# Performance work log

Hardware: AMD Instinct MI355X
Metric: run time of the kernel (lower is better)

The kernel has to match this reference:

```python
import jax, jax.numpy as jnp
import numpy as np

N = 50000            # num nodes
E = 800000           # num edges
IN_CH = 128          # memory_dim (node feature dim)
OUT_CH = 128         # out_channels (4 heads x 32)
HEADS = 4
HEAD_DIM = OUT_CH // HEADS
TIME_DIM = 100
MSG_DIM = 1
EDGE_DIM = TIME_DIM + MSG_DIM
T_MAX = 1_000_000


def _glorot(k, shape):
    lim = (6.0 / (shape[0] + shape[1])) ** 0.5
    return jax.random.uniform(k, shape, jnp.float32, -lim, lim)


def setup_inputs() -> dict:
    key = jax.random.key(0)
    ks = jax.random.split(key, 16)
    return {
        "x": jax.random.normal(ks[0], (N, IN_CH), jnp.float32),
        "msg": jax.random.normal(ks[1], (E, MSG_DIM), jnp.float32),
        # TimeEncoder: Linear(1, time_dim) followed by cos
        "Wt": _glorot(ks[2], (1, TIME_DIM)),
        "bt": jnp.zeros((TIME_DIM,), jnp.float32),
        # TransformerConv projections (stored [in, out])
        "Wq": _glorot(ks[3], (IN_CH, OUT_CH)),
        "bq": jnp.zeros((OUT_CH,), jnp.float32),
        "Wk": _glorot(ks[4], (IN_CH, OUT_CH)),
        "bk": jnp.zeros((OUT_CH,), jnp.float32),
        "Wv": _glorot(ks[5], (IN_CH, OUT_CH)),
        "bv": jnp.zeros((OUT_CH,), jnp.float32),
        "We": _glorot(ks[6], (EDGE_DIM, OUT_CH)),   # lin_edge, bias=False
        "Wskip": _glorot(ks[7], (IN_CH, OUT_CH)),    # lin_skip (root weight)
        "bskip": jnp.zeros((OUT_CH,), jnp.float32),
        # LayerNorm params
        "gamma": jnp.ones((OUT_CH,), jnp.float32),
        "beta": jnp.zeros((OUT_CH,), jnp.float32),
        # int inputs
        "last_update": jax.random.randint(ks[8], (N,), 0, T_MAX, jnp.int64 if jax.config.jax_enable_x64 else jnp.int32),
        "edge_index": jax.random.randint(ks[9], (2, E), 0, N, jnp.int32),
        "t": jax.random.randint(ks[10], (E,), 0, T_MAX, jnp.int64 if jax.config.jax_enable_x64 else jnp.int32),
    }


def reference(x, msg, Wt, bt, Wq, bq, Wk, bk, Wv, bv, We, Wskip, bskip, gamma, beta,
              last_update, edge_index, t):
    src, dst = edge_index[0], edge_index[1]  # PyG: row=source j, col=target i

    # edge features: cos-time encoding of relative time, concat raw message
    rel_t = (last_update[src] - t).astype(jnp.float32)[:, None]        # [E,1]
    rel_t_enc = jnp.cos(rel_t @ Wt + bt)                               # [E,time_dim]
    edge_attr = jnp.concatenate([rel_t_enc, msg], axis=-1)             # [E,edge_dim]

    # TransformerConv (heads=4, per-head dim=32, concat=True, root_weight=True)
    q = (x @ Wq + bq)[dst].reshape(E, HEADS, HEAD_DIM)
    k = (x @ Wk + bk)[src].reshape(E, HEADS, HEAD_DIM)
    v = (x @ Wv + bv)[src].reshape(E, HEADS, HEAD_DIM)
    e = (edge_attr @ We).reshape(E, HEADS, HEAD_DIM)

    kj = k + e
    alpha = jnp.einsum('ehd,ehd->eh', q, kj) / jnp.sqrt(jnp.float32(HEAD_DIM))  # [E,H]

    # segment (scatter) softmax over incoming edges of each destination node
    m = jax.lax.stop_gradient(jax.ops.segment_max(alpha, dst, num_segments=N))  # [N,H]
    ea = jnp.exp(alpha - m[dst])
    den = jax.ops.segment_sum(ea, dst, num_segments=N)                          # [N,H]
    a = ea / (den[dst] + 1e-16)                                                  # [E,H]

    msg_e = (v + e) * a[..., None]                                               # [E,H,D]
    agg = jax.ops.segment_sum(msg_e.reshape(E, OUT_CH), dst, num_segments=N)     # [N,out]

    out = agg + (x @ Wskip + bskip)   # skip / root weight
    out = jax.nn.relu(out)

    # LayerNorm
    mu = out.mean(-1, keepdims=True)
    var = out.var(-1, keepdims=True)
    return (out - mu) * jax.lax.rsqrt(var + 1e-5) * gamma + beta
```

## Files before the change

### kernel.cpp

```cpp
#include <hip/hip_runtime.h>
#include <math.h>

#define NN 50000
#define NE 800000
#define TDIM 100
#define MAXCH 100000
#define NBLK 196

typedef _Float16 half2v __attribute__((ext_vector_type(2)));
typedef _Float16 half4v __attribute__((ext_vector_type(4)));
typedef _Float16 half8v __attribute__((ext_vector_type(8)));
typedef __fp16 fp16x2 __attribute__((ext_vector_type(2)));
typedef float f32x4 __attribute__((ext_vector_type(4)));

union U16 { uint4 u; half8v h; };
union U4h { unsigned u; half2v h; };

__device__ __forceinline__ float ref_cosf(float x) {
  const float C1 = 0.15915494f;
  const float C2 = 6.42063831e-9f;
  float p = x * C1;
  float r = __fmaf_rn(x, C1, -p);
  r = __fmaf_rn(x, C2, r);
  float n = rintf(p);
  float f = (p - n) + r;
  return __builtin_amdgcn_cosf(f);
}

__device__ __forceinline__ unsigned pk16(float a, float b) {
  fp16x2 h = __builtin_amdgcn_cvt_pkrtz(a, b);
  unsigned u;
  __builtin_memcpy(&u, &h, 4);
  return u;
}

__device__ __forceinline__ float fdot2f(unsigned a, unsigned b, float c) {
  U4h ua, ub; ua.u = a; ub.u = b;
#if __has_builtin(__builtin_amdgcn_fdot2)
  return __builtin_amdgcn_fdot2(ua.h, ub.h, c, false);
#else
  return c + (float)ua.h.x * (float)ub.h.x + (float)ua.h.y * (float)ub.h.y;
#endif
}

__device__ __forceinline__ unsigned pkadd(unsigned a, unsigned b) {
  half2v x, y; __builtin_memcpy(&x, &a, 4); __builtin_memcpy(&y, &b, 4);
  half2v z = x + y; unsigned r; __builtin_memcpy(&r, &z, 4); return r;
}
__device__ __forceinline__ unsigned pkmul(unsigned a, unsigned b) {
  half2v x, y; __builtin_memcpy(&x, &a, 4); __builtin_memcpy(&y, &b, 4);
  half2v z = x * y; unsigned r; __builtin_memcpy(&r, &z, 4); return r;
}

template<int CTRL>
__device__ __forceinline__ int dpp_i(int x) {
  return __builtin_amdgcn_update_dpp(0, x, CTRL, 0xf, 0xf, true);
}
template<int CTRL>
__device__ __forceinline__ float dpp_addf(float x) {
  return x + __int_as_float(dpp_i<CTRL>(__float_as_int(x)));
}
template<int CTRL>
__device__ __forceinline__ float dpp_maxf(float x) {
  return fmaxf(x, __int_as_float(dpp_i<CTRL>(__float_as_int(x))));
}
__device__ __forceinline__ float red16_add(float x) {
  x = dpp_addf<0xB1>(x); x = dpp_addf<0x4E>(x);
  x = dpp_addf<0x141>(x); x = dpp_addf<0x140>(x);
  return x;
}
__device__ __forceinline__ float red16_max(float x) {
  x = dpp_maxf<0xB1>(x); x = dpp_maxf<0x4E>(x);
  x = dpp_maxf<0x141>(x); x = dpp_maxf<0x140>(x);
  return x;
}
__device__ __forceinline__ unsigned red16_pkadd(unsigned x) {
  x = pkadd(x, (unsigned)dpp_i<0xB1>((int)x));
  x = pkadd(x, (unsigned)dpp_i<0x4E>((int)x));
  x = pkadd(x, (unsigned)dpp_i<0x141>((int)x));
  x = pkadd(x, (unsigned)dpp_i<0x140>((int)x));
  return x;
}

__device__ __forceinline__ void build_bfu(float rel_b, float mg_b, int g,
                                          const float2* wtbt_s, unsigned bfu[4][4]) {
#pragma unroll
  for (int ks = 0; ks < 4; ++ks) {
#pragma unroll
    for (int p = 0; p < 4; ++p) {
      int j0 = ks * 32 + g * 8 + 2 * p;
      float a0 = 0.f, a1 = 0.f;
      if (ks < 3) {
        float2 w0 = wtbt_s[j0], w1 = wtbt_s[j0 + 1];
        a0 = ref_cosf(__fmaf_rn(rel_b, w0.x, w0.y));
        a1 = ref_cosf(__fmaf_rn(rel_b, w1.x, w1.y));
      } else {
        if (j0 < 100) {
          float2 w0 = wtbt_s[j0];
          a0 = ref_cosf(__fmaf_rn(rel_b, w0.x, w0.y));
        } else if (j0 == 100) a0 = mg_b;
        if (j0 + 1 < 100) {
          float2 w1 = wtbt_s[j0 + 1];
          a1 = ref_cosf(__fmaf_rn(rel_b, w1.x, w1.y));
        } else if (j0 + 1 == 100) a1 = mg_b;
      }
      bfu[ks][p] = pk16(a0, a1);
    }
  }
}

__global__ void k_init(const float* __restrict__ We,
                       const float* __restrict__ Wq, const float* __restrict__ Wk,
                       const float* __restrict__ Wv, const float* __restrict__ Wskip,
                       uint4* __restrict__ wef, uint4* __restrict__ wpf,
                       const int* __restrict__ ei, int* __restrict__ deg) {
  int idx = blockIdx.x * 256 + threadIdx.x;
  if (idx < 2048) {
    int lane = idx & 63, fi = idx >> 6;
    int ks = fi >> 3, mt = fi & 7;
    int ch = mt * 16 + (lane & 15);
    int k0 = ks * 32 + ((lane >> 4) << 3);
    U16 cv;
#pragma unroll
    for (int jj = 0; jj < 8; ++jj) {
      int j = k0 + jj;
      cv.h[jj] = (j <= 100) ? (_Float16)We[j * 128 + ch] : (_Float16)0.f;
    }
    wef[idx] = cv.u;
  } else if (idx < 2048 + 8192) {
    int i2 = idx - 2048;
    int lane = i2 & 63, fi = i2 >> 6;
    int nt = fi & 7, ks = (fi >> 3) & 3, cy = fi >> 5;
    const float* W = (cy == 0) ? Wq : (cy == 1) ? Wk : (cy == 2) ? Wv : Wskip;
    int n = nt * 16 + (lane & 15);
    int k0 = ks * 32 + ((lane >> 4) << 3);
    U16 cv;
#pragma unroll
    for (int jj = 0; jj < 8; ++jj)
      cv.h[jj] = (_Float16)W[(k0 + jj) * 128 + n];
    wpf[i2] = cv.u;
  }
  if (idx < NE) atomicAdd(&deg[ei[NE + idx]], 1);
}

__global__ __launch_bounds__(256) void k_proj2(
    const float* __restrict__ x,
    const float* __restrict__ bq, const float* __restrict__ bk,
    const float* __restrict__ bv, const float* __restrict__ bskip,
    const uint4* __restrict__ wpf,
    _Float16* __restrict__ Q16, _Float16* __restrict__ K16,
    _Float16* __restrict__ V16, _Float16* __restrict__ S16)
{
  __shared__ unsigned xs[32][68];
  __shared__ _Float16 os[32][136];

  const int cy = blockIdx.x;
  const int n0 = blockIdx.y * 32;
  const int tid = threadIdx.x;
  const float* bias = (cy == 0) ? bq : (cy == 1) ? bk : (cy == 2) ? bv : bskip;
  _Float16* dst     = (cy == 0) ? Q16 : (cy == 1) ? K16 : (cy == 2) ? V16 : S16;

  {
    int r = tid >> 3, c16 = (tid & 7) * 16;
    int row = n0 + r;
    float4 v0 = {0,0,0,0}, v1 = {0,0,0,0}, v2 = {0,0,0,0}, v3 = {0,0,0,0};
    if (row < NN) {
      const float4* xp = (const float4*)&x[(size_t)row * 128 + c16];
      v0 = xp[0]; v1 = xp[1]; v2 = xp[2]; v3 = xp[3];
    }
    unsigned* xr = &xs[r][c16 >> 1];
    xr[0] = pk16(v0.x, v0.y); xr[1] = pk16(v0.z, v0.w);
    xr[2] = pk16(v1.x, v1.y); xr[3] = pk16(v1.z, v1.w);
    xr[4] = pk16(v2.x, v2.y); xr[5] = pk16(v2.z, v2.w);
    xr[6] = pk16(v3.x, v3.y); xr[7] = pk16(v3.z, v3.w);
  }
  __syncthreads();

  const int w = tid >> 6, lane = tid & 63;
  const int mrow = (w & 1) << 4;
  const int nh = w >> 1;

  f32x4 acc[4] = {{0,0,0,0},{0,0,0,0},{0,0,0,0},{0,0,0,0}};
#pragma unroll
  for (int ks = 0; ks < 4; ++ks) {
    U16 a_; a_.u = *(const uint4*)&xs[mrow + (lane & 15)][ks * 16 + ((lane >> 4) << 2)];
#pragma unroll
    for (int nt = 0; nt < 4; ++nt) {
      U16 b_; b_.u = wpf[((cy * 4 + ks) * 8 + nh * 4 + nt) * 64 + lane];
      acc[nt] = __builtin_amdgcn_mfma_f32_16x16x32_f16(a_.h, b_.h, acc[nt], 0, 0, 0);
    }
  }

#pragma unroll
  for (int nt = 0; nt < 4; ++nt) {
    int col = (nh * 4 + nt) * 16 + (lane & 15);
    float bb = bias[col];
    int rbase = mrow + ((lane >> 4) << 2);
#pragma unroll
    for (int reg = 0; reg < 4; ++reg)
      os[rbase + reg][col] = (_Float16)(acc[nt][reg] + bb);
  }
  __syncthreads();

  {
    int r = tid >> 3, c16 = (tid & 7) * 16;
    int row = n0 + r;
    if (row < NN) {
      const _Float16* op = &os[r][c16];
      if (cy < 3) {
#pragma unroll
        for (int q = 0; q < 4; ++q) {
          int j4 = (c16 >> 2) + q;
          int po = ((j4 & 3) << 5) | ((j4 >> 2) << 2);
          *(half4v*)&dst[(size_t)row * 128 + po] = *(const half4v*)&op[q * 4];
        }
      } else {
        *(uint4*)&dst[(size_t)row * 128 + c16]     = ((const uint4*)op)[0];
        *(uint4*)&dst[(size_t)row * 128 + c16 + 8] = ((const uint4*)op)[1];
      }
    }
  }
}

__global__ __launch_bounds__(256) void k_scan1(const int* __restrict__ deg,
                                               int* __restrict__ off,
                                               int* __restrict__ choff,
                                               int* __restrict__ bsum,
                                               int* __restrict__ bsumc) {
  __shared__ int s[256], sc[256];
  const int b = blockIdx.x, t = threadIdx.x;
  const int n = b * 256 + t;
  int d = (n < NN) ? deg[n] : 0;
  int c = (d + 15) >> 4;
  s[t] = d; sc[t] = c;
  __syncthreads();
  for (int o = 1; o < 256; o <<= 1) {
    int v1 = 0, v2 = 0;
    if (t >= o) { v1 = s[t - o]; v2 = sc[t - o]; }
    __syncthreads();
    if (t >= o) { s[t] += v1; sc[t] += v2; }
    __syncthreads();
  }
  if (n < NN) { off[n] = s[t] - d; choff[n] = sc[t] - c; }
  if (t == 255) { bsum[b] = s[255]; bsumc[b] = sc[255]; }
}

__global__ __launch_bounds__(256) void k_scan2(int* __restrict__ bsum,
                                               int* __restrict__ bsumc,
                                               int* __restrict__ off,
                                               int* __restrict__ choff) {
  __shared__ int s[256], sc[256];
  const int t = threadIdx.x;
  int v = (t < NBLK) ? bsum[t] : 0;
  int vc = (t < NBLK) ? bsumc[t] : 0;
  s[t] = v; sc[t] = vc;
  __syncthreads();
  for (int o = 1; o < 256; o <<= 1) {
    int v1 = 0, v2 = 0;
    if (t >= o) { v1 = s[t - o]; v2 = sc[t - o]; }
    __syncthreads();
    if (t >= o) { s[t] += v1; sc[t] += v2; }
    __syncthreads();
  }
  if (t < NBLK) { bsum[t] = s[t] - v; bsumc[t] = sc[t] - vc; }
  if (t == 255) { off[NN] = s[255]; choff[NN] = sc[255]; }
}

__global__ void k_scan3(int* __restrict__ off, int* __restrict__ choff,
                        const int* __restrict__ bsum, const int* __restrict__ bsumc) {
  int b = blockIdx.x, n = b * 256 + threadIdx.x;
  if (n < NN) { off[n] += bsum[b]; choff[n] += bsumc[b]; }
}

__global__ void k_fillch(const int* __restrict__ ei, const int* __restrict__ deg,
                         const int* __restrict__ off, const int* __restrict__ choff,
                         int* __restrict__ cur, int* __restrict__ elist,
                         uint2* __restrict__ chunks) {
  int b = blockIdx.x;
  if (b < 3125) {
    int e = b * 256 + threadIdx.x;
    if (e < NE) {
      int d = ei[NE + e];
      int p = atomicAdd(&cur[d], 1);
      elist[off[d] + p] = e;
    }
  } else {
    int n = (b - 3125) * 256 + threadIdx.x;
    if (n < NN) {
      int d = deg[n], o = off[n], c = choff[n];
      int nch = (d + 15) >> 4;
      for (int j = 0; j < nch; ++j) {
        int cnt = d - 16 * j; if (cnt > 16) cnt = 16;
        chunks[c + j] = make_uint2((unsigned)(o + 16 * j),
                                   ((unsigned)n << 5) | (unsigned)cnt);
      }
    }
  }
}

__global__ __launch_bounds__(512) void k_edge(
    const _Float16* __restrict__ Q16, const _Float16* __restrict__ K16,
    const _Float16* __restrict__ V16,
    const float* __restrict__ Wt, const float* __restrict__ bt,
    const uint4* __restrict__ wefrag,
    const float* __restrict__ msg, const int* __restrict__ last_update,
    const int* __restrict__ ei, const int* __restrict__ tt,
    const int* __restrict__ elist, const uint2* __restrict__ chunks,
    const int* __restrict__ choff,
    unsigned* __restrict__ numbuf, float4* __restrict__ mdm,
    float4* __restrict__ mdd)
{
  __shared__ uint4 wef_s[2048];
  __shared__ float2 wtbt_s[104];
  __shared__ unsigned accs_u[8][64];

  for (int i = threadIdx.x; i < 2048; i += 512) wef_s[i] = wefrag[i];
  if (threadIdx.x < 104) {
    int j = threadIdx.x;
    wtbt_s[j] = make_float2(j < TDIM ? Wt[j] : 0.f, j < TDIM ? bt[j] : 0.f);
  }
  __syncthreads();

  const int wid = threadIdx.x >> 6, lane = threadIdx.x & 63;
  const int chunk = blockIdx.x * 8 + wid;
  if (chunk >= choff[NN]) return;

  uint2 ce = chunks[chunk];
  const int estart = (int)ce.x;
  const int node = (int)(ce.y >> 5);
  const int cnt = (int)(ce.y & 31u);
  const int g = lane >> 4, ed = lane & 15;

  const int edc = (ed < cnt) ? ed : (cnt - 1);
  const int eid = elist[estart + edc];
  const int src_b = ei[eid];
  const float mg_b = msg[eid];
  const float rel_b = (float)(last_update[src_b] - tt[eid]);
  const bool valid = (ed < cnt);

  unsigned bfu[4][4];
  build_bfu(rel_b, mg_b, g, wtbt_s, bfu);

  f32x4 ec[8];
#pragma unroll
  for (int mt = 0; mt < 8; ++mt) {
    f32x4 c4 = {0.f, 0.f, 0.f, 0.f};
#pragma unroll
    for (int ks = 0; ks < 4; ++ks) {
      U16 av2; av2.u = wef_s[(ks * 8 + mt) * 64 + lane];
      U16 bv2; bv2.u.x = bfu[ks][0]; bv2.u.y = bfu[ks][1];
      bv2.u.z = bfu[ks][2]; bv2.u.w = bfu[ks][3];
      c4 = __builtin_amdgcn_mfma_f32_16x16x32_f16(av2.h, bv2.h, c4, 0, 0, 0);
    }
    ec[mt] = c4;
  }

  unsigned ep2[16];
#pragma unroll
  for (int mt = 0; mt < 8; ++mt) {
    ep2[mt * 2 + 0] = pk16(ec[mt][0], ec[mt][1]);
    ep2[mt * 2 + 1] = pk16(ec[mt][2], ec[mt][3]);
  }

  float pal[4];
  {
    const uint4* qp = (const uint4*)&Q16[(size_t)node * 128 + g * 32];
    const uint4* kp = (const uint4*)&K16[(size_t)src_b * 128 + g * 32];
#pragma unroll
    for (int i = 0; i < 4; ++i) {
      uint4 qa = qp[i], ka = kp[i];
      float p = 0.f;
      p = fdot2f(qa.x, ka.x, p); p = fdot2f(qa.y, ka.y, p);
      p = fdot2f(qa.z, ka.z, p); p = fdot2f(qa.w, ka.w, p);
      p = fdot2f(qa.x, ep2[4 * i + 0], p); p = fdot2f(qa.y, ep2[4 * i + 1], p);
      p = fdot2f(qa.z, ep2[4 * i + 2], p); p = fdot2f(qa.w, ep2[4 * i + 3], p);
      pal[i] = p;
    }
  }

  float m_[4], w_[4], d_[4];
#pragma unroll
  for (int h = 0; h < 4; ++h) {
    float p = pal[h];
    p += __shfl_xor(p, 16); p += __shfl_xor(p, 32);
    float al = valid ? p * 0.17677669529663689f : -INFINITY;
    float mm = red16_max(al);
    m_[h] = mm;
    w_[h] = __expf(al - mm);
    d_[h] = red16_add(w_[h]);
  }

  unsigned np2[16];
  {
    const uint4* vp = (const uint4*)&V16[(size_t)src_b * 128 + g * 32];
#pragma unroll
    for (int i = 0; i < 4; ++i) {
      uint4 va = vp[i];
      unsigned w2 = pk16(w_[i], w_[i]);
      np2[4 * i + 0] = pkmul(pkadd(va.x, ep2[4 * i + 0]), w2);
      np2[4 * i + 1] = pkmul(pkadd(va.y, ep2[4 * i + 1]), w2);
      np2[4 * i + 2] = pkmul(pkadd(va.z, ep2[4 * i + 2]), w2);
      np2[4 * i + 3] = pkmul(pkadd(va.w, ep2[4 * i + 3]), w2);
    }
  }
#pragma unroll
  for (int j = 0; j < 16; ++j) np2[j] = red16_pkadd(np2[j]);

  if (ed == 0) {
#pragma unroll
    for (int i = 0; i < 4; ++i)
#pragma unroll
      for (int j = 0; j < 4; ++j)
        accs_u[wid][16 * i + 8 * (j >> 1) + 2 * g + (j & 1)] = np2[4 * i + j];
  }
  __asm__ volatile("s_waitcnt lgkmcnt(0)" ::: "memory");

  numbuf[(size_t)chunk * 64 + lane] = accs_u[wid][lane];
  if (lane == 0) {
    mdm[chunk] = make_float4(m_[0], m_[1], m_[2], m_[3]);
    mdd[chunk] = make_float4(d_[0], d_[1], d_[2], d_[3]);
  }
}

__global__ __launch_bounds__(256) void k_comb(
    const unsigned* __restrict__ numbuf, const float* __restrict__ mdmf,
    const float* __restrict__ mddf, const _Float16* __restrict__ S16,
    const float* __restrict__ gamma, const float* __restrict__ beta,
    const int* __restrict__ choff, float* __restrict__ out)
{
  const int wid = threadIdx.x >> 6, lane = threadIdx.x & 63;
  const int node = blockIdx.x * 4 + wid;
  const int g = lane >> 4;
  const int c0 = choff[node], c1 = choff[node + 1];

  float M = -INFINITY;
  for (int c = c0; c < c1; ++c) M = fmaxf(M, mdmf[c * 4 + g]);

  float den = 0.f, n0 = 0.f, n1 = 0.f;
  for (int c = c0; c < c1; ++c) {
    float sc = __expf(mdmf[c * 4 + g] - M);
    den = fmaf(mddf[c * 4 + g], sc, den);
    U4h u; u.u = numbuf[(size_t)c * 64 + lane];
    n0 = fmaf((float)u.h.x, sc, n0);
    n1 = fmaf((float)u.h.y, sc, n1);
  }

  float iv = 1.f / (den + 1e-16f);
  U4h s2; s2.u = *(const unsigned*)&S16[(size_t)node * 128 + 2 * lane];
  float r0 = fmaxf(fmaf(n0, iv, (float)s2.h.x), 0.f);
  float r1 = fmaxf(fmaf(n1, iv, (float)s2.h.y), 0.f);

  float sum = r0 + r1;
#pragma unroll
  for (int o = 1; o < 64; o <<= 1) sum += __shfl_xor(sum, o);
  float mu = sum * 0.0078125f;
  float d0 = r0 - mu, d1 = r1 - mu;
  float vs = d0 * d0 + d1 * d1;
#pragma unroll
  for (int o = 1; o < 64; o <<= 1) vs += __shfl_xor(vs, o);
  float rstd = rsqrtf(vs * 0.0078125f + 1e-5f);
  float2 gm = ((const float2*)gamma)[lane], bb = ((const float2*)beta)[lane];
  ((float2*)out)[node * 64 + lane] =
      make_float2(d0 * rstd * gm.x + bb.x, d1 * rstd * gm.y + bb.y);
}

extern "C" void kernel_launch(void* const* d_in, const int* in_sizes, int n_in,
                              void* d_out, int out_size, void* d_ws, size_t ws_size,
                              hipStream_t stream)
{
  (void)in_sizes; (void)n_in; (void)out_size;
  if (ws_size < 84965968u) return;

  const float* x     = (const float*)d_in[0];
  const float* msg   = (const float*)d_in[1];
  const float* Wt    = (const float*)d_in[2];
  const float* bt    = (const float*)d_in[3];
  const float* Wq    = (const float*)d_in[4];
  const float* bq    = (const float*)d_in[5];
  const float* Wk    = (const float*)d_in[6];
  const float* bk    = (const float*)d_in[7];
  const float* Wv    = (const float*)d_in[8];
  const float* bv    = (const float*)d_in[9];
  const float* We    = (const float*)d_in[10];
  const float* Wskip = (const float*)d_in[11];
  const float* bskip = (const float*)d_in[12];
  const float* gamma = (const float*)d_in[13];
  const float* beta  = (const float*)d_in[14];
  const int* last_update = (const int*)d_in[15];
  const int* ei    = (const int*)d_in[16];
  const int* tt    = (const int*)d_in[17];

  char* ws = (char*)d_ws;
  _Float16* Q16 = (_Float16*)(ws);
  _Float16* S16 = (_Float16*)(ws + 12800000);
  _Float16* K16 = (_Float16*)(ws + 25600000);
  _Float16* V16 = (_Float16*)(ws + 38400000);
  unsigned* numbuf = (unsigned*)(ws + 51200000);
  int* deg   = (int*)(ws + 76800000);
  int* cur   = (int*)(ws + 77000000);
  int* off   = (int*)(ws + 77200000);
  int* choff = (int*)(ws + 77400064);
  int* elist = (int*)(ws + 77600128);
  uint4* wef = (uint4*)(ws + 80800128);
  uint2* chunks = (uint2*)(ws + 80832896);
  float4* mdm = (float4*)(ws + 81632896);
  float4* mdd = (float4*)(ws + 83232896);
  uint4* wpf = (uint4*)(ws + 84832896);
  int* bsum  = (int*)(ws + 84963968);
  int* bsumc = (int*)(ws + 84964968);

  (void)hipMemsetAsync(deg, 0, 400000, stream);
  k_init<<<(NE + 255) / 256, 256, 0, stream>>>(We, Wq, Wk, Wv, Wskip, wef, wpf,
                                               ei, deg);
  k_scan1<<<NBLK, 256, 0, stream>>>(deg, off, choff, bsum, bsumc);
  k_scan2<<<1, 256, 0, stream>>>(bsum, bsumc, off, choff);
  k_scan3<<<NBLK, 256, 0, stream>>>(off, choff, bsum, bsumc);
  k_fillch<<<3125 + (NN + 255) / 256, 256, 0, stream>>>(ei, deg, off, choff,
                                                        cur, elist, chunks);
  dim3 pg(4, (NN + 31) / 32);
  k_proj2<<<pg, 256, 0, stream>>>(x, bq, bk, bv, bskip, wpf,
                                  Q16, K16, V16, S16);
  k_edge<<<MAXCH / 8, 512, 0, stream>>>(Q16, K16, V16, Wt, bt, wef,
                                        msg, last_update, ei, tt, elist,
                                        chunks, choff, numbuf, mdm, mdd);
  k_comb<<<NN / 4, 256, 0, stream>>>(numbuf, (const float*)mdm, (const float*)mdd,
                                     S16, gamma, beta, choff, (float*)d_out);
}
```

Before: 276.4 us.

## Fuse projection blocks per row tile, merge scan kernels, early-exit idle edge blocks

The projection kernel now runs one 512-thread block per 32-row tile that computes all four projections (Q, K, V, skip). Each row of x is loaded and converted to fp16 once instead of four times, and outputs are staged through shared memory projection by projection. The scan2 and scan3 kernels are merged into one multi-block kernel where every block redoes the small block-sum scan, which removes one launch. The edge kernel now checks the chunk count before loading weights into shared memory, so surplus blocks exit without that work. The costs are extra barriers in the projection epilogue and redundant per-block scan work.

```diff
diff --git a/kernel.cpp b/kernel.cpp
--- a/kernel.cpp
+++ b/kernel.cpp
@@ -143,7 +143,7 @@
   if (idx < NE) atomicAdd(&deg[ei[NE + idx]], 1);
 }
 
-__global__ __launch_bounds__(256) void k_proj2(
+__global__ __launch_bounds__(512) void k_proj2(
     const float* __restrict__ x,
     const float* __restrict__ bq, const float* __restrict__ bk,
     const float* __restrict__ bv, const float* __restrict__ bskip,
@@ -154,69 +154,75 @@
   __shared__ unsigned xs[32][68];
   __shared__ _Float16 os[32][136];
 
-  const int cy = blockIdx.x;
-  const int n0 = blockIdx.y * 32;
+  const int n0 = blockIdx.x * 32;
   const int tid = threadIdx.x;
-  const float* bias = (cy == 0) ? bq : (cy == 1) ? bk : (cy == 2) ? bv : bskip;
-  _Float16* dst     = (cy == 0) ? Q16 : (cy == 1) ? K16 : (cy == 2) ? V16 : S16;
 
   {
-    int r = tid >> 3, c16 = (tid & 7) * 16;
+    int r = tid >> 4, c8 = (tid & 15) * 8;
     int row = n0 + r;
-    float4 v0 = {0,0,0,0}, v1 = {0,0,0,0}, v2 = {0,0,0,0}, v3 = {0,0,0,0};
+    float4 v0 = {0,0,0,0}, v1 = {0,0,0,0};
     if (row < NN) {
-      const float4* xp = (const float4*)&x[(size_t)row * 128 + c16];
-      v0 = xp[0]; v1 = xp[1]; v2 = xp[2]; v3 = xp[3];
-    }
-    unsigned* xr = &xs[r][c16 >> 1];
+      const float4* xp = (const float4*)&x[(size_t)row * 128 + c8];
+      v0 = xp[0]; v1 = xp[1];
+    }
+    unsigned* xr = &xs[r][c8 >> 1];
     xr[0] = pk16(v0.x, v0.y); xr[1] = pk16(v0.z, v0.w);
     xr[2] = pk16(v1.x, v1.y); xr[3] = pk16(v1.z, v1.w);
-    xr[4] = pk16(v2.x, v2.y); xr[5] = pk16(v2.z, v2.w);
-    xr[6] = pk16(v3.x, v3.y); xr[7] = pk16(v3.z, v3.w);
   }
   __syncthreads();
 
   const int w = tid >> 6, lane = tid & 63;
-  const int mrow = (w & 1) << 4;
-  const int nh = w >> 1;
-
-  f32x4 acc[4] = {{0,0,0,0},{0,0,0,0},{0,0,0,0},{0,0,0,0}};
+  const int cy = w >> 1, half = w & 1;
+
+  f32x4 acc[2][4] = {};
 #pragma unroll
   for (int ks = 0; ks < 4; ++ks) {
-    U16 a_; a_.u = *(const uint4*)&xs[mrow + (lane & 15)][ks * 16 + ((lane >> 4) << 2)];
+    U16 a0_, a1_;
+    a0_.u = *(const uint4*)&xs[lane & 15][ks * 16 + ((lane >> 4) << 2)];
+    a1_.u = *(const uint4*)&xs[16 + (lane & 15)][ks * 16 + ((lane >> 4) << 2)];
 #pragma unroll
     for (int nt = 0; nt < 4; ++nt) {
-      U16 b_; b_.u = wpf[((cy * 4 + ks) * 8 + nh * 4 + nt) * 64 + lane];
-      acc[nt] = __builtin_amdgcn_mfma_f32_16x16x32_f16(a_.h, b_.h, acc[nt], 0, 0, 0);
-    }
-  }
-
-#pragma unroll
-  for (int nt = 0; nt < 4; ++nt) {
-    int col = (nh * 4 + nt) * 16 + (lane & 15);
-    float bb = bias[col];
-    int rbase = mrow + ((lane >> 4) << 2);
-#pragma unroll
-    for (int reg = 0; reg < 4; ++reg)
-      os[rbase + reg][col] = (_Float16)(acc[nt][reg] + bb);
-  }
-  __syncthreads();
-
-  {
-    int r = tid >> 3, c16 = (tid & 7) * 16;
-    int row = n0 + r;
-    if (row < NN) {
-      const _Float16* op = &os[r][c16];
-      if (cy < 3) {
-#pragma unroll
-        for (int q = 0; q < 4; ++q) {
-          int j4 = (c16 >> 2) + q;
-          int po = ((j4 & 3) << 5) | ((j4 >> 2) << 2);
-          *(half4v*)&dst[(size_t)row * 128 + po] = *(const half4v*)&op[q * 4];
+      U16 b_; b_.u = wpf[((cy * 4 + ks) * 8 + half * 4 + nt) * 64 + lane];
+      acc[0][nt] = __builtin_amdgcn_mfma_f32_16x16x32_f16(a0_.h, b_.h, acc[0][nt], 0, 0, 0);
+      acc[1][nt] = __builtin_amdgcn_mfma_f32_16x16x32_f16(a1_.h, b_.h, acc[1][nt], 0, 0, 0);
+    }
+  }
+
+  const float* biases[4] = {bq, bk, bv, bskip};
+  _Float16* dsts[4] = {Q16, K16, V16, S16};
+#pragma unroll
+  for (int c = 0; c < 4; ++c) {
+    __syncthreads();
+    if (cy == c) {
+#pragma unroll
+      for (int nt = 0; nt < 4; ++nt) {
+        int col = half * 64 + nt * 16 + (lane & 15);
+        float bb = biases[c][col];
+        int rb = (lane >> 4) << 2;
+#pragma unroll
+        for (int mt2 = 0; mt2 < 2; ++mt2)
+#pragma unroll
+          for (int reg = 0; reg < 4; ++reg)
+            os[mt2 * 16 + rb + reg][col] = (_Float16)(acc[mt2][nt][reg] + bb);
+      }
+    }
+    __syncthreads();
+    {
+      int r = tid >> 4, c8 = (tid & 15) * 8;
+      int row = n0 + r;
+      if (row < NN) {
+        _Float16* dst = dsts[c];
+        const _Float16* op = &os[r][c8];
+        if (c < 3) {
+#pragma unroll
+          for (int q = 0; q < 2; ++q) {
+            int j4 = (c8 >> 2) + q;
+            int po = ((j4 & 3) << 5) | ((j4 >> 2) << 2);
+            *(half4v*)&dst[(size_t)row * 128 + po] = *(const half4v*)&op[q * 4];
+          }
+        } else {
+          *(uint4*)&dst[(size_t)row * 128 + c8] = *((const uint4*)op);
         }
-      } else {
-        *(uint4*)&dst[(size_t)row * 128 + c16]     = ((const uint4*)op)[0];
-        *(uint4*)&dst[(size_t)row * 128 + c16 + 8] = ((const uint4*)op)[1];
       }
     }
   }
@@ -245,15 +251,14 @@
   if (t == 255) { bsum[b] = s[255]; bsumc[b] = sc[255]; }
 }
 
-__global__ __launch_bounds__(256) void k_scan2(int* __restrict__ bsum,
-                                               int* __restrict__ bsumc,
+__global__ __launch_bounds__(256) void k_scanf(const int* __restrict__ bsum,
+                                               const int* __restrict__ bsumc,
                                                int* __restrict__ off,
                                                int* __restrict__ choff) {
   __shared__ int s[256], sc[256];
-  const int t = threadIdx.x;
-  int v = (t < NBLK) ? bsum[t] : 0;
-  int vc = (t < NBLK) ? bsumc[t] : 0;
-  s[t] = v; sc[t] = vc;
+  const int b = blockIdx.x, t = threadIdx.x;
+  s[t] = (t < NBLK) ? bsum[t] : 0;
+  sc[t] = (t < NBLK) ? bsumc[t] : 0;
   __syncthreads();
   for (int o = 1; o < 256; o <<= 1) {
     int v1 = 0, v2 = 0;
@@ -262,14 +267,11 @@
     if (t >= o) { s[t] += v1; sc[t] += v2; }
     __syncthreads();
   }
-  if (t < NBLK) { bsum[t] = s[t] - v; bsumc[t] = sc[t] - vc; }
-  if (t == 255) { off[NN] = s[255]; choff[NN] = sc[255]; }
-}
-
-__global__ void k_scan3(int* __restrict__ off, int* __restrict__ choff,
-                        const int* __restrict__ bsum, const int* __restrict__ bsumc) {
-  int b = blockIdx.x, n = b * 256 + threadIdx.x;
-  if (n < NN) { off[n] += bsum[b]; choff[n] += bsumc[b]; }
+  int base = (b > 0) ? s[b - 1] : 0;
+  int basec = (b > 0) ? sc[b - 1] : 0;
+  int n = b * 256 + t;
+  if (n < NN) { off[n] += base; choff[n] += basec; }
+  if (b == 0 && t == 0) { off[NN] = s[NBLK - 1]; choff[NN] = sc[NBLK - 1]; }
 }
 
 __global__ void k_fillch(const int* __restrict__ ei, const int* __restrict__ deg,
@@ -314,6 +316,9 @@
   __shared__ float2 wtbt_s[104];
   __shared__ unsigned accs_u[8][64];
 
+  const int nchunks = choff[NN];
+  if (blockIdx.x * 8 >= nchunks) return;
+
   for (int i = threadIdx.x; i < 2048; i += 512) wef_s[i] = wefrag[i];
   if (threadIdx.x < 104) {
     int j = threadIdx.x;
@@ -323,7 +328,7 @@
 
   const int wid = threadIdx.x >> 6, lane = threadIdx.x & 63;
   const int chunk = blockIdx.x * 8 + wid;
-  if (chunk >= choff[NN]) return;
+  if (chunk >= nchunks) return;
 
   uint2 ce = chunks[chunk];
   const int estart = (int)ce.x;
@@ -513,13 +518,11 @@
   k_init<<<(NE + 255) / 256, 256, 0, stream>>>(We, Wq, Wk, Wv, Wskip, wef, wpf,
                                                ei, deg);
   k_scan1<<<NBLK, 256, 0, stream>>>(deg, off, choff, bsum, bsumc);
-  k_scan2<<<1, 256, 0, stream>>>(bsum, bsumc, off, choff);
-  k_scan3<<<NBLK, 256, 0, stream>>>(off, choff, bsum, bsumc);
+  k_scanf<<<NBLK, 256, 0, stream>>>(bsum, bsumc, off, choff);
   k_fillch<<<3125 + (NN + 255) / 256, 256, 0, stream>>>(ei, deg, off, choff,
                                                         cur, elist, chunks);
-  dim3 pg(4, (NN + 31) / 32);
-  k_proj2<<<pg, 256, 0, stream>>>(x, bq, bk, bv, bskip, wpf,
-                                  Q16, K16, V16, S16);
+  k_proj2<<<(NN + 31) / 32, 512, 0, stream>>>(x, bq, bk, bv, bskip, wpf,
+                                              Q16, K16, V16, S16);
   k_edge<<<MAXCH / 8, 512, 0, stream>>>(Q16, K16, V16, Wt, bt, wef,
                                         msg, last_update, ei, tt, elist,
                                         chunks, choff, numbuf, mdm, mdd);
```

Result: no change. 274.5 us (-0.7%).
